# Optimization experiments

Hardware: AMD Instinct MI355X
Metric: run time of the kernel (lower is better)

The kernel has to match this reference:

```python
import jax, jax.numpy as jnp
from jax import lax
import numpy as np

GZ = 15.0   # grid extent (float, from gz=15.0)
G = 15      # grid cells per axis


def _disty(p):
    # p: [B, N, 3] points in [0, GZ). 12 features per point:
    # offsets to cell center / lower corner / upper corner (9) + their euclidean norms (3)
    c = jnp.floor(jnp.clip(p, 0.0, GZ - 1e-4))
    off_c = p - (c + 0.5)
    off_l = p - c
    off_u = p - (c + 1.0)
    norms = jnp.stack([jnp.sqrt((o * o).sum(-1)) for o in (off_c, off_l, off_u)], axis=-1)
    return jnp.concatenate([off_c, off_l, off_u, norms], axis=-1)  # [B, N, 12]


def _mlp(x, W1, b1, W2, b2, W3, b3):
    h = jax.nn.elu(x @ W1 + b1)
    h = jax.nn.elu(h @ W2 + b2)
    return h @ W3 + b3  # [B, N, 4]


def _agg(feats, p):
    # scatter-max per-point features into the [G,G,G] grid of each scene
    B, N, C = feats.shape
    cell = jnp.floor(jnp.clip(p, 0.0, GZ - 1e-4)).astype(jnp.int32)  # [B, N, 3]
    flat = (cell[..., 0] * G + cell[..., 1]) * G + cell[..., 2]
    flat = flat + (jnp.arange(B, dtype=jnp.int32) * (G ** 3))[:, None]
    grid = jnp.zeros((B * G ** 3, C), feats.dtype)
    grid = grid.at[flat.reshape(-1)].max(feats.reshape(-1, C))
    return grid.reshape(B, G, G, G, C).transpose(0, 4, 1, 2, 3)  # [B, 4, G, G, G]


def _conv_bn_elu(x, w, b, g, beta, stride):
    y = lax.conv_general_dilated(x, w, (stride,) * 3, [(2, 2)] * 3,
                                 dimension_numbers=('NCDHW', 'OIDHW', 'NCDHW'))
    y = y + b[None, :, None, None, None]
    # BatchNorm3d, training mode (batch statistics), eps=1e-5
    m = y.mean((0, 2, 3, 4), keepdims=True)
    v = ((y - m) ** 2).mean((0, 2, 3, 4), keepdims=True)
    y = (y - m) * lax.rsqrt(v + 1e-5)
    y = y * g[None, :, None, None, None] + beta[None, :, None, None, None]
    return jax.nn.elu(y)


def setup_inputs():
    key = jax.random.key(0)
    ks = jax.random.split(key, 16)
    B, N = 4, 300000
    pts = lambda k: jax.random.uniform(k, (B, N, 3), jnp.float32, 0.0, GZ)
    lin = lambda k, i, o: (jax.random.normal(k, (i, o), jnp.float32) / np.sqrt(i)).astype(jnp.float32)
    inp = {
        'goals': pts(ks[0]), 'inputs': pts(ks[1]), 'backgrounds': pts(ks[2]),
        'W1': lin(ks[3], 12, 16), 'b1': jnp.zeros((16,), jnp.float32),
        'W2': lin(ks[4], 16, 16), 'b2': jnp.zeros((16,), jnp.float32),
        'W3': lin(ks[5], 16, 4),  'b3': jnp.zeros((4,), jnp.float32),
        'conv1_w': (jax.random.normal(ks[6], (8, 12, 5, 5, 5), jnp.float32) / np.sqrt(12 * 125)).astype(jnp.float32),
        'conv1_b': jnp.zeros((8,), jnp.float32),
        'bn1_g': jnp.ones((8,), jnp.float32), 'bn1_b': jnp.zeros((8,), jnp.float32),
        'convs_w': (jax.random.normal(ks[7], (6, 8, 8, 5, 5, 5), jnp.float32) / np.sqrt(8 * 125)).astype(jnp.float32),
        'convs_b': jnp.zeros((6, 8), jnp.float32),
        'bns_g': jnp.ones((6, 8), jnp.float32), 'bns_b': jnp.zeros((6, 8), jnp.float32),
    }
    return inp


def reference(goals, inputs, backgrounds, W1, b1, W2, b2, W3, b3,
              conv1_w, conv1_b, bn1_g, bn1_b, convs_w, convs_b, bns_g, bns_b):
    def encode(p):
        return _agg(_mlp(_disty(p), W1, b1, W2, b2, W3, b3), p)

    scenes = jnp.concatenate([encode(inputs), encode(goals), encode(backgrounds)], axis=1)  # [B,12,G,G,G]
    x = _conv_bn_elu(scenes, conv1_w, conv1_b, bn1_g, bn1_b, 2)  # [B,8,8,8,8]
    for i in range(6):
        x = _conv_bn_elu(x, convs_w[i], convs_b[i], bns_g[i], bns_b[i], 1)
    return x
```

## Files before the change

kernel.cpp:

```cpp
#include <hip/hip_runtime.h>
#include <math.h>

#define B 4
#define NPTS 300000
#define G 15
#define G3 3375
#define PAIR_FLOATS (4*G3)
#define SCENE_FLOATS (B*12*G3)

__device__ __forceinline__ float eluf(float v) {
    return v > 0.0f ? v : __expf(v) - 1.0f;
}

__global__ __launch_bounds__(256)
void mlp_kernel(const float* __restrict__ P0,
                const float* __restrict__ P1,
                const float* __restrict__ P2,
                const float* __restrict__ W1, const float* __restrict__ b1,
                const float* __restrict__ W2, const float* __restrict__ b2,
                const float* __restrict__ W3, const float* __restrict__ b3,
                float4* __restrict__ vals, int* __restrict__ cells,
                int s0, int m)
{
    int b   = blockIdx.y;
    int set = blockIdx.z;
    int i   = blockIdx.x * 256 + threadIdx.x;
    if (i >= m) return;
    const float* P = (set == 0) ? P0 : ((set == 1) ? P1 : P2);

    const float* p = P + ((size_t)b * NPTS + (size_t)(s0 + i)) * 3;
    float px = p[0], py = p[1], pz = p[2];

    const float HI = 14.9999f;
    float cx = floorf(fminf(fmaxf(px, 0.0f), HI));
    float cy = floorf(fminf(fmaxf(py, 0.0f), HI));
    float cz = floorf(fminf(fmaxf(pz, 0.0f), HI));

    float x[12];
    x[0] = px - (cx + 0.5f); x[1] = py - (cy + 0.5f); x[2] = pz - (cz + 0.5f);
    x[3] = px - cx;          x[4] = py - cy;          x[5] = pz - cz;
    x[6] = px - (cx + 1.0f); x[7] = py - (cy + 1.0f); x[8] = pz - (cz + 1.0f);
    x[9]  = sqrtf(x[0]*x[0] + x[1]*x[1] + x[2]*x[2]);
    x[10] = sqrtf(x[3]*x[3] + x[4]*x[4] + x[5]*x[5]);
    x[11] = sqrtf(x[6]*x[6] + x[7]*x[7] + x[8]*x[8]);

    float h1[16];
#pragma unroll
    for (int j = 0; j < 16; ++j) {
        float s = b1[j];
#pragma unroll
        for (int k = 0; k < 12; ++k) s = fmaf(x[k], W1[k*16 + j], s);
        h1[j] = eluf(s);
    }
    float h2[16];
#pragma unroll
    for (int j = 0; j < 16; ++j) {
        float s = b2[j];
#pragma unroll
        for (int k = 0; k < 16; ++k) s = fmaf(h1[k], W2[k*16 + j], s);
        h2[j] = eluf(s);
    }
    float o[4];
#pragma unroll
    for (int j = 0; j < 4; ++j) {
        float s = b3[j];
#pragma unroll
        for (int k = 0; k < 16; ++k) s = fmaf(h2[k], W3[k*4 + j], s);
        o[j] = s;
    }

    int cell = (((int)cx) * G + (int)cy) * G + (int)cz;
    int pair = b * 3 + set;
    vals [(size_t)pair * m + i] = make_float4(o[0], o[1], o[2], o[3]);
    cells[(size_t)pair * m + i] = cell;
}

__global__ __launch_bounds__(256)
void scatter_kernel(const float4* __restrict__ vals,
                    const int* __restrict__ cells,
                    float* __restrict__ scenesR, int K, int m, int carry)
{
    __shared__ unsigned sg[PAIR_FLOATS];

    int rep = blockIdx.x;
    int b   = blockIdx.y;
    int set = blockIdx.z;
    int pair = b * 3 + set;
    float* myrep = scenesR + ((size_t)pair * K + rep) * PAIR_FLOATS;

    if (carry) {
        for (int i = threadIdx.x; i < PAIR_FLOATS; i += 256)
            sg[i] = __float_as_uint(myrep[i]);
    } else {
        for (int i = threadIdx.x; i < PAIR_FLOATS; i += 256)
            sg[i] = 0u;
    }
    __syncthreads();

    int chunk = (m + K - 1) / K;
    int start = rep * chunk;
    int end   = min(m, start + chunk);
    const float4* v = vals  + (size_t)pair * m;
    const int*    c = cells + (size_t)pair * m;

    for (int i = start + (int)threadIdx.x; i < end; i += 256) {
        float4 o = v[i];
        int cell = c[i];
        if (o.x > 0.0f) atomicMax(&sg[          cell], __float_as_uint(o.x));
        if (o.y > 0.0f) atomicMax(&sg[    G3 + cell], __float_as_uint(o.y));
        if (o.z > 0.0f) atomicMax(&sg[2 * G3 + cell], __float_as_uint(o.z));
        if (o.w > 0.0f) atomicMax(&sg[3 * G3 + cell], __float_as_uint(o.w));
    }
    __syncthreads();

    for (int i = threadIdx.x; i < PAIR_FLOATS; i += 256)
        myrep[i] = __uint_as_float(sg[i]);
}

__global__ __launch_bounds__(256)
void reduce_kernel(const float* __restrict__ scenesR, float* __restrict__ scenes,
                   int K)
{
    int t = blockIdx.x * 256 + threadIdx.x;
    if (t >= SCENE_FLOATS) return;
    int pair = t / PAIR_FLOATS;
    int j    = t - pair * PAIR_FLOATS;
    const float* src = scenesR + (size_t)pair * K * PAIR_FLOATS + j;
    float mx = 0.0f;
    for (int r = 0; r < K; ++r)
        mx = fmaxf(mx, src[(size_t)r * PAIR_FLOATS]);
    scenes[t] = mx;
}

__global__ __launch_bounds__(256)
void conv1_kernel(const float* __restrict__ scenes,
                  const float* __restrict__ w,
                  const float* __restrict__ bias,
                  float* __restrict__ y, float* __restrict__ stats)
{
    __shared__ float sred[256];
    int bx = blockIdx.x;
    int od = bx & 7, co = (bx >> 3) & 7, b = bx >> 6;
    int tid = threadIdx.x;
    int ow = tid & 7, oh = (tid >> 3) & 7, ciq = tid >> 6;

    float s = 0.0f;
    for (int cin = 0; cin < 3; ++cin) {
        int ci = ciq * 3 + cin;
        const float* sc = scenes + (size_t)(b * 12 + ci) * G3;
        const float* wc = w + (size_t)(co * 12 + ci) * 125;
#pragma unroll
        for (int kd = 0; kd < 5; ++kd) {
            int id = od * 2 - 2 + kd;
            if ((unsigned)id >= (unsigned)G) continue;
#pragma unroll
            for (int kh = 0; kh < 5; ++kh) {
                int ih = oh * 2 - 2 + kh;
                bool hok = (unsigned)ih < (unsigned)G;
#pragma unroll
                for (int kw = 0; kw < 5; ++kw) {
                    int iw = ow * 2 - 2 + kw;
                    if (hok && (unsigned)iw < (unsigned)G)
                        s = fmaf(sc[(id * G + ih) * G + iw], wc[kd*25 + kh*5 + kw], s);
                }
            }
        }
    }
    sred[tid] = s;
    __syncthreads();
    if (tid < 64) {
        float tot = sred[tid] + sred[64+tid] + sred[128+tid] + sred[192+tid] + bias[co];
        y[(size_t)(b * 8 + co) * 512 + od * 64 + tid] = tot;
        float sum = tot, sq = tot * tot;
#pragma unroll
        for (int o = 32; o > 0; o >>= 1) {
            sum += __shfl_down(sum, o, 64);
            sq  += __shfl_down(sq,  o, 64);
        }
        if (tid == 0) { atomicAdd(&stats[co], sum); atomicAdd(&stats[8 + co], sq); }
    }
}

__global__ __launch_bounds__(256)
void conv_s_kernel(const float* __restrict__ yin,
                   const float* __restrict__ w,
                   const float* __restrict__ bias,
                   const float* __restrict__ g, const float* __restrict__ bet,
                   const float* __restrict__ stats_in,
                   float* __restrict__ yout, float* __restrict__ stats_out)
{
    __shared__ float slab[8 * 5 * 144];
    __shared__ float sscale[8], sshift[8];
    __shared__ float sred[256];

    int bx = blockIdx.x;
    int od = bx & 7, co = (bx >> 3) & 7, b = bx >> 6;
    int tid = threadIdx.x;

    if (tid < 8) {
        float S = stats_in[tid], Q = stats_in[8 + tid];
        float m  = S * (1.0f / 2048.0f);
        float vv = Q * (1.0f / 2048.0f) - m * m;
        float rs = rsqrtf(vv + 1e-5f);
        float sc = g[tid] * rs;
        sscale[tid] = sc;
        sshift[tid] = bet[tid] - m * sc;
    }
    __syncthreads();

    for (int s = tid; s < 5760; s += 256) {
        int ci = s / 720; int r = s % 720;
        int kd = r / 144; int r2 = r % 144;
        int ph = r2 / 12, pw = r2 % 12;
        int id = od - 2 + kd, ih = ph - 2, iw = pw - 2;
        float v = 0.0f;
        if ((unsigned)id < 8u && (unsigned)ih < 8u && (unsigned)iw < 8u) {
            float raw = yin[(size_t)(b * 8 + ci) * 512 + id * 64 + ih * 8 + iw];
            float t = fmaf(raw, sscale[ci], sshift[ci]);
            v = t > 0.0f ? t : __expf(t) - 1.0f;
        }
        slab[s] = v;
    }
    __syncthreads();

    int ow = tid & 7, oh = (tid >> 3) & 7, ciq = tid >> 6;
    float s = 0.0f;
#pragma unroll
    for (int c2 = 0; c2 < 2; ++c2) {
        int ci = ciq * 2 + c2;
        const float* sl = slab + ci * 720;
        const float* wc = w + (size_t)(co * 8 + ci) * 125;
#pragma unroll
        for (int kd = 0; kd < 5; ++kd) {
#pragma unroll
            for (int kh = 0; kh < 5; ++kh) {
                const float* row = sl + kd * 144 + (oh + kh) * 12 + ow;
                const float* wr = wc + kd * 25 + kh * 5;
#pragma unroll
                for (int kw = 0; kw < 5; ++kw) s = fmaf(row[kw], wr[kw], s);
            }
        }
    }
    sred[tid] = s;
    __syncthreads();
    if (tid < 64) {
        float tot = sred[tid] + sred[64+tid] + sred[128+tid] + sred[192+tid] + bias[co];
        yout[(size_t)(b * 8 + co) * 512 + od * 64 + tid] = tot;
        float sum = tot, sq = tot * tot;
#pragma unroll
        for (int o = 32; o > 0; o >>= 1) {
            sum += __shfl_down(sum, o, 64);
            sq  += __shfl_down(sq,  o, 64);
        }
        if (tid == 0) { atomicAdd(&stats_out[co], sum); atomicAdd(&stats_out[8 + co], sq); }
    }
}

__global__ __launch_bounds__(256)
void bn_final_kernel(const float* __restrict__ yin,
                     const float* __restrict__ g, const float* __restrict__ bet,
                     const float* __restrict__ stats_in, float* __restrict__ outp)
{
    int i = blockIdx.x * 256 + threadIdx.x;
    int c = (i >> 9) & 7;
    float S = stats_in[c], Q = stats_in[8 + c];
    float m  = S * (1.0f / 2048.0f);
    float vv = Q * (1.0f / 2048.0f) - m * m;
    float rs = rsqrtf(vv + 1e-5f);
    float sc = g[c] * rs;
    float sh = bet[c] - m * sc;
    float t = fmaf(yin[i], sc, sh);
    outp[i] = t > 0.0f ? t : __expf(t) - 1.0f;
}

extern "C" void kernel_launch(void* const* d_in, const int* in_sizes, int n_in,
                              void* d_out, int out_size, void* d_ws, size_t ws_size,
                              hipStream_t stream)
{
    const float* goals       = (const float*)d_in[0];
    const float* inputs      = (const float*)d_in[1];
    const float* backgrounds = (const float*)d_in[2];
    const float* W1 = (const float*)d_in[3];
    const float* b1 = (const float*)d_in[4];
    const float* W2 = (const float*)d_in[5];
    const float* b2 = (const float*)d_in[6];
    const float* W3 = (const float*)d_in[7];
    const float* b3 = (const float*)d_in[8];
    const float* conv1_w = (const float*)d_in[9];
    const float* conv1_b = (const float*)d_in[10];
    const float* bn1_g   = (const float*)d_in[11];
    const float* bn1_b   = (const float*)d_in[12];
    const float* convs_w = (const float*)d_in[13];
    const float* convs_b = (const float*)d_in[14];
    const float* bns_g   = (const float*)d_in[15];
    const float* bns_b   = (const float*)d_in[16];

    long ws_floats = (long)(ws_size / 4);
    long fixed = SCENE_FLOATS + 2L * 16384 + 112;
    static const int plans[][2] = {
        {42,1},{42,2},{42,4},{24,4},{21,6},{16,8},{8,12},{4,16},{2,32},{1,64}};
    int K = 1, S = 64;
    for (int pi = 0; pi < 10; ++pi) {
        int pk = plans[pi][0], ps = plans[pi][1];
        long mseg = (NPTS + ps - 1) / ps;
        long need = 60L * mseg + (long)pk * SCENE_FLOATS + fixed;
        if (need <= ws_floats) { K = pk; S = ps; break; }
    }
    int Mseg = (NPTS + S - 1) / S;

    float*  wsp     = (float*)d_ws;
    float4* vals    = (float4*)wsp;
    int*    cells   = (int*)(wsp + 48L * Mseg);
    float*  scenesR = wsp + 60L * Mseg;
    float*  scenes  = scenesR + (size_t)K * SCENE_FLOATS;
    float*  yA      = scenes + SCENE_FLOATS;
    float*  yB      = yA + 16384;
    float*  stats   = yB + 16384;

    hipMemsetAsync(stats, 0, 7 * 16 * sizeof(float), stream);

    for (int s = 0; s < S; ++s) {
        int s0 = s * Mseg;
        int m  = min(Mseg, NPTS - s0);
        dim3 agrid((m + 255) / 256, B, 3);
        mlp_kernel<<<agrid, 256, 0, stream>>>(inputs, goals, backgrounds,
                                              W1, b1, W2, b2, W3, b3,
                                              vals, cells, s0, m);
        dim3 bgrid(K, B, 3);
        scatter_kernel<<<bgrid, 256, 0, stream>>>(vals, cells, scenesR, K, m,
                                                  s > 0 ? 1 : 0);
    }

    reduce_kernel<<<(SCENE_FLOATS + 255) / 256, 256, 0, stream>>>(scenesR, scenes, K);

    conv1_kernel<<<256, 256, 0, stream>>>(scenes, conv1_w, conv1_b, yA, stats);

    const float* cur = yA;
    float* nxt = yB;
    for (int i = 0; i < 6; ++i) {
        const float* g   = (i == 0) ? bn1_g : (bns_g + (i - 1) * 8);
        const float* bet = (i == 0) ? bn1_b : (bns_b + (i - 1) * 8);
        conv_s_kernel<<<256, 256, 0, stream>>>(
            cur, convs_w + (size_t)i * 8000, convs_b + i * 8,
            g, bet, stats + i * 16, nxt, stats + (i + 1) * 16);
        const float* tmp = cur; cur = nxt; nxt = (float*)tmp;
    }

    bn_final_kernel<<<64, 256, 0, stream>>>(cur, bns_g + 5 * 8, bns_b + 5 * 8,
                                            stats + 6 * 16, (float*)d_out);
}
```

Measured before the change: 327.4 us.

## Fuse reduce, conv chain and final BN into one cooperative kernel

Replaces the reduce, conv1, six conv_s and final BN launches with a single cooperative kernel that uses grid-wide syncs between stages. This removes about eight kernel launches and their inter-kernel gaps on the small tail of the pipeline. It relies on all 256 blocks being co-resident, and grid.sync costs stand in for the launch boundaries. The MLP/scatter stage, which dominates the runtime, is unchanged.

```diff
diff --git a/kernel.cpp b/kernel.cpp
--- a/kernel.cpp
+++ b/kernel.cpp
@@ -1,5 +1,8 @@
 #include <hip/hip_runtime.h>
+#include <hip/hip_cooperative_groups.h>
 #include <math.h>
+
+namespace cg = cooperative_groups;
 
 #define B 4
 #define NPTS 300000
@@ -118,159 +121,162 @@
 }
 
 __global__ __launch_bounds__(256)
-void reduce_kernel(const float* __restrict__ scenesR, float* __restrict__ scenes,
-                   int K)
+void conv_chain_kernel(const float* __restrict__ scenesR, float* __restrict__ scenes,
+                       const float* __restrict__ c1w,
+                       const float* __restrict__ c1b,
+                       const float* __restrict__ csw,
+                       const float* __restrict__ csb,
+                       const float* __restrict__ bn1_g, const float* __restrict__ bn1_b,
+                       const float* __restrict__ bns_g, const float* __restrict__ bns_b,
+                       float* __restrict__ yA, float* __restrict__ yB,
+                       float* __restrict__ stats, float* __restrict__ outp, int K)
 {
-    int t = blockIdx.x * 256 + threadIdx.x;
-    if (t >= SCENE_FLOATS) return;
-    int pair = t / PAIR_FLOATS;
-    int j    = t - pair * PAIR_FLOATS;
-    const float* src = scenesR + (size_t)pair * K * PAIR_FLOATS + j;
-    float mx = 0.0f;
-    for (int r = 0; r < K; ++r)
-        mx = fmaxf(mx, src[(size_t)r * PAIR_FLOATS]);
-    scenes[t] = mx;
-}
-
-__global__ __launch_bounds__(256)
-void conv1_kernel(const float* __restrict__ scenes,
-                  const float* __restrict__ w,
-                  const float* __restrict__ bias,
-                  float* __restrict__ y, float* __restrict__ stats)
-{
-    __shared__ float sred[256];
-    int bx = blockIdx.x;
-    int od = bx & 7, co = (bx >> 3) & 7, b = bx >> 6;
-    int tid = threadIdx.x;
-    int ow = tid & 7, oh = (tid >> 3) & 7, ciq = tid >> 6;
-
-    float s = 0.0f;
-    for (int cin = 0; cin < 3; ++cin) {
-        int ci = ciq * 3 + cin;
-        const float* sc = scenes + (size_t)(b * 12 + ci) * G3;
-        const float* wc = w + (size_t)(co * 12 + ci) * 125;
-#pragma unroll
-        for (int kd = 0; kd < 5; ++kd) {
-            int id = od * 2 - 2 + kd;
-            if ((unsigned)id >= (unsigned)G) continue;
-#pragma unroll
-            for (int kh = 0; kh < 5; ++kh) {
-                int ih = oh * 2 - 2 + kh;
-                bool hok = (unsigned)ih < (unsigned)G;
-#pragma unroll
-                for (int kw = 0; kw < 5; ++kw) {
-                    int iw = ow * 2 - 2 + kw;
-                    if (hok && (unsigned)iw < (unsigned)G)
-                        s = fmaf(sc[(id * G + ih) * G + iw], wc[kd*25 + kh*5 + kw], s);
-                }
-            }
-        }
-    }
-    sred[tid] = s;
-    __syncthreads();
-    if (tid < 64) {
-        float tot = sred[tid] + sred[64+tid] + sred[128+tid] + sred[192+tid] + bias[co];
-        y[(size_t)(b * 8 + co) * 512 + od * 64 + tid] = tot;
-        float sum = tot, sq = tot * tot;
-#pragma unroll
-        for (int o = 32; o > 0; o >>= 1) {
-            sum += __shfl_down(sum, o, 64);
-            sq  += __shfl_down(sq,  o, 64);
-        }
-        if (tid == 0) { atomicAdd(&stats[co], sum); atomicAdd(&stats[8 + co], sq); }
-    }
-}
-
-__global__ __launch_bounds__(256)
-void conv_s_kernel(const float* __restrict__ yin,
-                   const float* __restrict__ w,
-                   const float* __restrict__ bias,
-                   const float* __restrict__ g, const float* __restrict__ bet,
-                   const float* __restrict__ stats_in,
-                   float* __restrict__ yout, float* __restrict__ stats_out)
-{
+    cg::grid_group gridg = cg::this_grid();
+
     __shared__ float slab[8 * 5 * 144];
     __shared__ float sscale[8], sshift[8];
     __shared__ float sred[256];
 
-    int bx = blockIdx.x;
+    int bx  = blockIdx.x;
+    int tid = threadIdx.x;
+    int gtid = bx * 256 + tid;
     int od = bx & 7, co = (bx >> 3) & 7, b = bx >> 6;
-    int tid = threadIdx.x;
-
-    if (tid < 8) {
-        float S = stats_in[tid], Q = stats_in[8 + tid];
+
+    for (int t = gtid; t < SCENE_FLOATS; t += 256 * 256) {
+        int pair = t / PAIR_FLOATS;
+        int j    = t - pair * PAIR_FLOATS;
+        const float* src = scenesR + (size_t)pair * K * PAIR_FLOATS + j;
+        float mx = 0.0f;
+        for (int r = 0; r < K; ++r)
+            mx = fmaxf(mx, src[(size_t)r * PAIR_FLOATS]);
+        scenes[t] = mx;
+    }
+    gridg.sync();
+
+    {
+        int ow = tid & 7, oh = (tid >> 3) & 7, ciq = tid >> 6;
+        float s = 0.0f;
+        for (int cin = 0; cin < 3; ++cin) {
+            int ci = ciq * 3 + cin;
+            const float* sc = scenes + (size_t)(b * 12 + ci) * G3;
+            const float* wc = c1w + (size_t)(co * 12 + ci) * 125;
+#pragma unroll
+            for (int kd = 0; kd < 5; ++kd) {
+                int id = od * 2 - 2 + kd;
+                if ((unsigned)id >= (unsigned)G) continue;
+#pragma unroll
+                for (int kh = 0; kh < 5; ++kh) {
+                    int ih = oh * 2 - 2 + kh;
+                    bool hok = (unsigned)ih < (unsigned)G;
+#pragma unroll
+                    for (int kw = 0; kw < 5; ++kw) {
+                        int iw = ow * 2 - 2 + kw;
+                        if (hok && (unsigned)iw < (unsigned)G)
+                            s = fmaf(sc[(id * G + ih) * G + iw], wc[kd*25 + kh*5 + kw], s);
+                    }
+                }
+            }
+        }
+        sred[tid] = s;
+        __syncthreads();
+        if (tid < 64) {
+            float tot = sred[tid] + sred[64+tid] + sred[128+tid] + sred[192+tid] + c1b[co];
+            yA[(size_t)(b * 8 + co) * 512 + od * 64 + tid] = tot;
+            float sum = tot, sq = tot * tot;
+#pragma unroll
+            for (int o = 32; o > 0; o >>= 1) {
+                sum += __shfl_down(sum, o, 64);
+                sq  += __shfl_down(sq,  o, 64);
+            }
+            if (tid == 0) { atomicAdd(&stats[co], sum); atomicAdd(&stats[8 + co], sq); }
+        }
+    }
+    gridg.sync();
+
+    float* cur = yA;
+    float* nxt = yB;
+    for (int layer = 0; layer < 6; ++layer) {
+        const float* g        = (layer == 0) ? bn1_g : (bns_g + (layer - 1) * 8);
+        const float* bet      = (layer == 0) ? bn1_b : (bns_b + (layer - 1) * 8);
+        const float* stats_in = stats + layer * 16;
+        float*      stats_out = stats + (layer + 1) * 16;
+        const float* w        = csw + (size_t)layer * 8000;
+        const float* bias     = csb + layer * 8;
+
+        if (tid < 8) {
+            float S = stats_in[tid], Q = stats_in[8 + tid];
+            float m  = S * (1.0f / 2048.0f);
+            float vv = Q * (1.0f / 2048.0f) - m * m;
+            float rs = rsqrtf(vv + 1e-5f);
+            float sc = g[tid] * rs;
+            sscale[tid] = sc;
+            sshift[tid] = bet[tid] - m * sc;
+        }
+        __syncthreads();
+
+        for (int s = tid; s < 5760; s += 256) {
+            int ci = s / 720; int r = s % 720;
+            int kd = r / 144; int r2 = r % 144;
+            int ph = r2 / 12, pw = r2 % 12;
+            int id = od - 2 + kd, ih = ph - 2, iw = pw - 2;
+            float v = 0.0f;
+            if ((unsigned)id < 8u && (unsigned)ih < 8u && (unsigned)iw < 8u) {
+                float raw = cur[(size_t)(b * 8 + ci) * 512 + id * 64 + ih * 8 + iw];
+                float t = fmaf(raw, sscale[ci], sshift[ci]);
+                v = t > 0.0f ? t : __expf(t) - 1.0f;
+            }
+            slab[s] = v;
+        }
+        __syncthreads();
+
+        int ow = tid & 7, oh = (tid >> 3) & 7, ciq = tid >> 6;
+        float s = 0.0f;
+#pragma unroll
+        for (int c2 = 0; c2 < 2; ++c2) {
+            int ci = ciq * 2 + c2;
+            const float* sl = slab + ci * 720;
+            const float* wc = w + (size_t)(co * 8 + ci) * 125;
+#pragma unroll
+            for (int kd = 0; kd < 5; ++kd) {
+#pragma unroll
+                for (int kh = 0; kh < 5; ++kh) {
+                    const float* row = sl + kd * 144 + (oh + kh) * 12 + ow;
+                    const float* wr = wc + kd * 25 + kh * 5;
+#pragma unroll
+                    for (int kw = 0; kw < 5; ++kw) s = fmaf(row[kw], wr[kw], s);
+                }
+            }
+        }
+        sred[tid] = s;
+        __syncthreads();
+        if (tid < 64) {
+            float tot = sred[tid] + sred[64+tid] + sred[128+tid] + sred[192+tid] + bias[co];
+            nxt[(size_t)(b * 8 + co) * 512 + od * 64 + tid] = tot;
+            float sum = tot, sq = tot * tot;
+#pragma unroll
+            for (int o = 32; o > 0; o >>= 1) {
+                sum += __shfl_down(sum, o, 64);
+                sq  += __shfl_down(sq,  o, 64);
+            }
+            if (tid == 0) { atomicAdd(&stats_out[co], sum); atomicAdd(&stats_out[8 + co], sq); }
+        }
+        gridg.sync();
+        float* tmp = cur; cur = nxt; nxt = tmp;
+        __syncthreads();
+    }
+
+    if (gtid < 16384) {
+        const float* stats_in = stats + 6 * 16;
+        int c = (gtid >> 9) & 7;
+        float S = stats_in[c], Q = stats_in[8 + c];
         float m  = S * (1.0f / 2048.0f);
         float vv = Q * (1.0f / 2048.0f) - m * m;
         float rs = rsqrtf(vv + 1e-5f);
-        float sc = g[tid] * rs;
-        sscale[tid] = sc;
-        sshift[tid] = bet[tid] - m * sc;
-    }
-    __syncthreads();
-
-    for (int s = tid; s < 5760; s += 256) {
-        int ci = s / 720; int r = s % 720;
-        int kd = r / 144; int r2 = r % 144;
-        int ph = r2 / 12, pw = r2 % 12;
-        int id = od - 2 + kd, ih = ph - 2, iw = pw - 2;
-        float v = 0.0f;
-        if ((unsigned)id < 8u && (unsigned)ih < 8u && (unsigned)iw < 8u) {
-            float raw = yin[(size_t)(b * 8 + ci) * 512 + id * 64 + ih * 8 + iw];
-            float t = fmaf(raw, sscale[ci], sshift[ci]);
-            v = t > 0.0f ? t : __expf(t) - 1.0f;
-        }
-        slab[s] = v;
-    }
-    __syncthreads();
-
-    int ow = tid & 7, oh = (tid >> 3) & 7, ciq = tid >> 6;
-    float s = 0.0f;
-#pragma unroll
-    for (int c2 = 0; c2 < 2; ++c2) {
-        int ci = ciq * 2 + c2;
-        const float* sl = slab + ci * 720;
-        const float* wc = w + (size_t)(co * 8 + ci) * 125;
-#pragma unroll
-        for (int kd = 0; kd < 5; ++kd) {
-#pragma unroll
-            for (int kh = 0; kh < 5; ++kh) {
-                const float* row = sl + kd * 144 + (oh + kh) * 12 + ow;
-                const float* wr = wc + kd * 25 + kh * 5;
-#pragma unroll
-                for (int kw = 0; kw < 5; ++kw) s = fmaf(row[kw], wr[kw], s);
-            }
-        }
-    }
-    sred[tid] = s;
-    __syncthreads();
-    if (tid < 64) {
-        float tot = sred[tid] + sred[64+tid] + sred[128+tid] + sred[192+tid] + bias[co];
-        yout[(size_t)(b * 8 + co) * 512 + od * 64 + tid] = tot;
-        float sum = tot, sq = tot * tot;
-#pragma unroll
-        for (int o = 32; o > 0; o >>= 1) {
-            sum += __shfl_down(sum, o, 64);
-            sq  += __shfl_down(sq,  o, 64);
-        }
-        if (tid == 0) { atomicAdd(&stats_out[co], sum); atomicAdd(&stats_out[8 + co], sq); }
-    }
-}
-
-__global__ __launch_bounds__(256)
-void bn_final_kernel(const float* __restrict__ yin,
-                     const float* __restrict__ g, const float* __restrict__ bet,
-                     const float* __restrict__ stats_in, float* __restrict__ outp)
-{
-    int i = blockIdx.x * 256 + threadIdx.x;
-    int c = (i >> 9) & 7;
-    float S = stats_in[c], Q = stats_in[8 + c];
-    float m  = S * (1.0f / 2048.0f);
-    float vv = Q * (1.0f / 2048.0f) - m * m;
-    float rs = rsqrtf(vv + 1e-5f);
-    float sc = g[c] * rs;
-    float sh = bet[c] - m * sc;
-    float t = fmaf(yin[i], sc, sh);
-    outp[i] = t > 0.0f ? t : __expf(t) - 1.0f;
+        float sc = (bns_g + 5 * 8)[c] * rs;
+        float sh = (bns_b + 5 * 8)[c] - m * sc;
+        float t = fmaf(cur[gtid], sc, sh);
+        outp[gtid] = t > 0.0f ? t : __expf(t) - 1.0f;
+    }
 }
 
 extern "C" void kernel_launch(void* const* d_in, const int* in_sizes, int n_in,
@@ -331,21 +337,12 @@
                                                   s > 0 ? 1 : 0);
     }
 
-    reduce_kernel<<<(SCENE_FLOATS + 255) / 256, 256, 0, stream>>>(scenesR, scenes, K);
-
-    conv1_kernel<<<256, 256, 0, stream>>>(scenes, conv1_w, conv1_b, yA, stats);
-
-    const float* cur = yA;
-    float* nxt = yB;
-    for (int i = 0; i < 6; ++i) {
-        const float* g   = (i == 0) ? bn1_g : (bns_g + (i - 1) * 8);
-        const float* bet = (i == 0) ? bn1_b : (bns_b + (i - 1) * 8);
-        conv_s_kernel<<<256, 256, 0, stream>>>(
-            cur, convs_w + (size_t)i * 8000, convs_b + i * 8,
-            g, bet, stats + i * 16, nxt, stats + (i + 1) * 16);
-        const float* tmp = cur; cur = nxt; nxt = (float*)tmp;
-    }
-
-    bn_final_kernel<<<64, 256, 0, stream>>>(cur, bns_g + 5 * 8, bns_b + 5 * 8,
-                                            stats + 6 * 16, (float*)d_out);
-}
+    float* outp = (float*)d_out;
+    void* cargs[] = {
+        (void*)&scenesR, (void*)&scenes, (void*)&conv1_w, (void*)&conv1_b,
+        (void*)&convs_w, (void*)&convs_b, (void*)&bn1_g, (void*)&bn1_b,
+        (void*)&bns_g, (void*)&bns_b, (void*)&yA, (void*)&yB,
+        (void*)&stats, (void*)&outp, (void*)&K };
+    hipLaunchCooperativeKernel((void*)conv_chain_kernel, dim3(256), dim3(256),
+                               cargs, 0, stream);
+}
```

Result: slower. 541.8 us (+65.5%).

## Fuse conv tail layers into persistent kernel with grid barrier; widen scatter blocks

Applied to the files above, without the earlier changes.

Replaces the six per-layer conv kernels and the final BN kernel with a single persistent 32-block kernel. Each block handles one (batch, out-channel) pair across all depths and syncs layers through an atomic grid barrier. This removes several kernel launches and the final elementwise pass. The cost is less parallelism per layer and a reliance on all blocks being co-resident. The scatter kernel block size is also doubled to 512 threads.

```diff
diff --git a/kernel.cpp b/kernel.cpp
--- a/kernel.cpp
+++ b/kernel.cpp
@@ -75,7 +75,7 @@
     cells[(size_t)pair * m + i] = cell;
 }
 
-__global__ __launch_bounds__(256)
+__global__ __launch_bounds__(512)
 void scatter_kernel(const float4* __restrict__ vals,
                     const int* __restrict__ cells,
                     float* __restrict__ scenesR, int K, int m, int carry)
@@ -89,10 +89,10 @@
     float* myrep = scenesR + ((size_t)pair * K + rep) * PAIR_FLOATS;
 
     if (carry) {
-        for (int i = threadIdx.x; i < PAIR_FLOATS; i += 256)
+        for (int i = threadIdx.x; i < PAIR_FLOATS; i += 512)
             sg[i] = __float_as_uint(myrep[i]);
     } else {
-        for (int i = threadIdx.x; i < PAIR_FLOATS; i += 256)
+        for (int i = threadIdx.x; i < PAIR_FLOATS; i += 512)
             sg[i] = 0u;
     }
     __syncthreads();
@@ -103,7 +103,7 @@
     const float4* v = vals  + (size_t)pair * m;
     const int*    c = cells + (size_t)pair * m;
 
-    for (int i = start + (int)threadIdx.x; i < end; i += 256) {
+    for (int i = start + (int)threadIdx.x; i < end; i += 512) {
         float4 o = v[i];
         int cell = c[i];
         if (o.x > 0.0f) atomicMax(&sg[          cell], __float_as_uint(o.x));
@@ -113,7 +113,7 @@
     }
     __syncthreads();
 
-    for (int i = threadIdx.x; i < PAIR_FLOATS; i += 256)
+    for (int i = threadIdx.x; i < PAIR_FLOATS; i += 512)
         myrep[i] = __uint_as_float(sg[i]);
 }
 
@@ -182,95 +182,142 @@
 }
 
 __global__ __launch_bounds__(256)
-void conv_s_kernel(const float* __restrict__ yin,
-                   const float* __restrict__ w,
-                   const float* __restrict__ bias,
-                   const float* __restrict__ g, const float* __restrict__ bet,
-                   const float* __restrict__ stats_in,
-                   float* __restrict__ yout, float* __restrict__ stats_out)
-{
-    __shared__ float slab[8 * 5 * 144];
-    __shared__ float sscale[8], sshift[8];
+void tail32_kernel(const float* __restrict__ yA, float* __restrict__ yB,
+                   float* __restrict__ yC,
+                   const float* __restrict__ csw,
+                   const float* __restrict__ csb,
+                   const float* __restrict__ bn1_g, const float* __restrict__ bn1_b,
+                   const float* __restrict__ bns_g, const float* __restrict__ bns_b,
+                   float* __restrict__ stats, unsigned* __restrict__ bar,
+                   float* __restrict__ outp)
+{
+    __shared__ float slab[8 * 12 * 144];
     __shared__ float sred[256];
-
-    int bx = blockIdx.x;
-    int od = bx & 7, co = (bx >> 3) & 7, b = bx >> 6;
+    __shared__ float sfinal[512];
+    __shared__ float sstat[16], sscale[8], sshift[8];
+
     int tid = threadIdx.x;
-
-    if (tid < 8) {
-        float S = stats_in[tid], Q = stats_in[8 + tid];
+    int bx  = blockIdx.x;
+    int co = bx & 7, b = bx >> 3;
+
+    const float* yin = yA;
+    float* yout = yB;
+    unsigned gen = 0;
+
+    for (int layer = 0; layer < 6; ++layer) {
+        const float* g   = (layer == 0) ? bn1_g : (bns_g + (layer - 1) * 8);
+        const float* bet = (layer == 0) ? bn1_b : (bns_b + (layer - 1) * 8);
+        const float* stats_in  = stats + layer * 16;
+        float*       stats_out = stats + (layer + 1) * 16;
+        const float* w = csw + (size_t)layer * 8000;
+
+        if (tid < 16)
+            sstat[tid] = __hip_atomic_load(stats_in + tid, __ATOMIC_RELAXED,
+                                           __HIP_MEMORY_SCOPE_AGENT);
+        for (int i = tid; i < 8 * 12 * 144; i += 256) slab[i] = 0.0f;
+        __syncthreads();
+        if (tid < 8) {
+            float S = sstat[tid], Q = sstat[8 + tid];
+            float m  = S * (1.0f / 2048.0f);
+            float vv = Q * (1.0f / 2048.0f) - m * m;
+            float rs = rsqrtf(vv + 1e-5f);
+            float sc = g[tid] * rs;
+            sscale[tid] = sc;
+            sshift[tid] = bet[tid] - m * sc;
+        }
+        __syncthreads();
+
+        for (int s = tid; s < 4096; s += 256) {
+            int ci = s >> 9, r = s & 511;
+            int id = r >> 6, ih = (r >> 3) & 7, iw = r & 7;
+            const float* src = yin + ((size_t)(b * 8 + ci) << 9) + r;
+            float raw = (layer == 0)
+                ? *src
+                : __hip_atomic_load(src, __ATOMIC_RELAXED, __HIP_MEMORY_SCOPE_AGENT);
+            float t = fmaf(raw, sscale[ci], sshift[ci]);
+            slab[ci * 1728 + (id + 2) * 144 + (ih + 2) * 12 + (iw + 2)] =
+                t > 0.0f ? t : __expf(t) - 1.0f;
+        }
+        __syncthreads();
+
+        int ow = tid & 7, oh = (tid >> 3) & 7, ciq = tid >> 6;
+        float sum_acc = 0.0f, sq_acc = 0.0f;
+        for (int od = 0; od < 8; ++od) {
+            float s = 0.0f;
+#pragma unroll
+            for (int c2 = 0; c2 < 2; ++c2) {
+                int ci = ciq * 2 + c2;
+                const float* sl = slab + ci * 1728 + od * 144;
+                const float* wc = w + (size_t)(co * 8 + ci) * 125;
+#pragma unroll
+                for (int kd = 0; kd < 5; ++kd) {
+#pragma unroll
+                    for (int kh = 0; kh < 5; ++kh) {
+                        const float* row = sl + kd * 144 + (oh + kh) * 12 + ow;
+                        const float* wr = wc + kd * 25 + kh * 5;
+#pragma unroll
+                        for (int kw = 0; kw < 5; ++kw) s = fmaf(row[kw], wr[kw], s);
+                    }
+                }
+            }
+            sred[tid] = s;
+            __syncthreads();
+            if (tid < 64) {
+                float tot = sred[tid] + sred[64+tid] + sred[128+tid] + sred[192+tid]
+                          + csb[layer * 8 + co];
+                sfinal[od * 64 + tid] = tot;
+                sum_acc += tot;
+                sq_acc  += tot * tot;
+                if (layer < 5)
+                    __hip_atomic_store(yout + ((size_t)(b * 8 + co) << 9) + od * 64 + tid,
+                                       tot, __ATOMIC_RELAXED, __HIP_MEMORY_SCOPE_AGENT);
+            }
+            __syncthreads();
+        }
+        if (tid < 64) {
+#pragma unroll
+            for (int o = 32; o > 0; o >>= 1) {
+                sum_acc += __shfl_down(sum_acc, o, 64);
+                sq_acc  += __shfl_down(sq_acc,  o, 64);
+            }
+            if (tid == 0) {
+                atomicAdd(stats_out + co, sum_acc);
+                atomicAdd(stats_out + 8 + co, sq_acc);
+            }
+        }
+
+        ++gen;
+        __syncthreads();
+        if (tid == 0) {
+            __hip_atomic_fetch_add(bar, 1u, __ATOMIC_ACQ_REL, __HIP_MEMORY_SCOPE_AGENT);
+            while (__hip_atomic_load(bar, __ATOMIC_ACQUIRE, __HIP_MEMORY_SCOPE_AGENT)
+                   < 32u * gen)
+                __builtin_amdgcn_s_sleep(2);
+        }
+        __syncthreads();
+
+        if (layer == 0) { yin = yB; yout = yC; }
+        else { float* t_ = yout; yout = (float*)yin; yin = t_; }
+    }
+
+    if (tid < 16)
+        sstat[tid] = __hip_atomic_load(stats + 6 * 16 + tid, __ATOMIC_RELAXED,
+                                       __HIP_MEMORY_SCOPE_AGENT);
+    __syncthreads();
+    if (tid < 64) {
+        float S = sstat[co], Q = sstat[8 + co];
         float m  = S * (1.0f / 2048.0f);
         float vv = Q * (1.0f / 2048.0f) - m * m;
         float rs = rsqrtf(vv + 1e-5f);
-        float sc = g[tid] * rs;
-        sscale[tid] = sc;
-        sshift[tid] = bet[tid] - m * sc;
-    }
-    __syncthreads();
-
-    for (int s = tid; s < 5760; s += 256) {
-        int ci = s / 720; int r = s % 720;
-        int kd = r / 144; int r2 = r % 144;
-        int ph = r2 / 12, pw = r2 % 12;
-        int id = od - 2 + kd, ih = ph - 2, iw = pw - 2;
-        float v = 0.0f;
-        if ((unsigned)id < 8u && (unsigned)ih < 8u && (unsigned)iw < 8u) {
-            float raw = yin[(size_t)(b * 8 + ci) * 512 + id * 64 + ih * 8 + iw];
-            float t = fmaf(raw, sscale[ci], sshift[ci]);
-            v = t > 0.0f ? t : __expf(t) - 1.0f;
-        }
-        slab[s] = v;
-    }
-    __syncthreads();
-
-    int ow = tid & 7, oh = (tid >> 3) & 7, ciq = tid >> 6;
-    float s = 0.0f;
-#pragma unroll
-    for (int c2 = 0; c2 < 2; ++c2) {
-        int ci = ciq * 2 + c2;
-        const float* sl = slab + ci * 720;
-        const float* wc = w + (size_t)(co * 8 + ci) * 125;
-#pragma unroll
-        for (int kd = 0; kd < 5; ++kd) {
-#pragma unroll
-            for (int kh = 0; kh < 5; ++kh) {
-                const float* row = sl + kd * 144 + (oh + kh) * 12 + ow;
-                const float* wr = wc + kd * 25 + kh * 5;
-#pragma unroll
-                for (int kw = 0; kw < 5; ++kw) s = fmaf(row[kw], wr[kw], s);
-            }
-        }
-    }
-    sred[tid] = s;
-    __syncthreads();
-    if (tid < 64) {
-        float tot = sred[tid] + sred[64+tid] + sred[128+tid] + sred[192+tid] + bias[co];
-        yout[(size_t)(b * 8 + co) * 512 + od * 64 + tid] = tot;
-        float sum = tot, sq = tot * tot;
-#pragma unroll
-        for (int o = 32; o > 0; o >>= 1) {
-            sum += __shfl_down(sum, o, 64);
-            sq  += __shfl_down(sq,  o, 64);
-        }
-        if (tid == 0) { atomicAdd(&stats_out[co], sum); atomicAdd(&stats_out[8 + co], sq); }
-    }
-}
-
-__global__ __launch_bounds__(256)
-void bn_final_kernel(const float* __restrict__ yin,
-                     const float* __restrict__ g, const float* __restrict__ bet,
-                     const float* __restrict__ stats_in, float* __restrict__ outp)
-{
-    int i = blockIdx.x * 256 + threadIdx.x;
-    int c = (i >> 9) & 7;
-    float S = stats_in[c], Q = stats_in[8 + c];
-    float m  = S * (1.0f / 2048.0f);
-    float vv = Q * (1.0f / 2048.0f) - m * m;
-    float rs = rsqrtf(vv + 1e-5f);
-    float sc = g[c] * rs;
-    float sh = bet[c] - m * sc;
-    float t = fmaf(yin[i], sc, sh);
-    outp[i] = t > 0.0f ? t : __expf(t) - 1.0f;
+        float sc = (bns_g + 5 * 8)[co] * rs;
+        float sh = (bns_b + 5 * 8)[co] - m * sc;
+#pragma unroll
+        for (int od = 0; od < 8; ++od) {
+            float t = fmaf(sfinal[od * 64 + tid], sc, sh);
+            outp[((size_t)(b * 8 + co) << 9) + od * 64 + tid] =
+                t > 0.0f ? t : __expf(t) - 1.0f;
+        }
+    }
 }
 
 extern "C" void kernel_launch(void* const* d_in, const int* in_sizes, int n_in,
@@ -296,7 +343,7 @@
     const float* bns_b   = (const float*)d_in[16];
 
     long ws_floats = (long)(ws_size / 4);
-    long fixed = SCENE_FLOATS + 2L * 16384 + 112;
+    long fixed = SCENE_FLOATS + 3L * 16384 + 128;
     static const int plans[][2] = {
         {42,1},{42,2},{42,4},{24,4},{21,6},{16,8},{8,12},{4,16},{2,32},{1,64}};
     int K = 1, S = 64;
@@ -308,16 +355,18 @@
     }
     int Mseg = (NPTS + S - 1) / S;
 
-    float*  wsp     = (float*)d_ws;
-    float4* vals    = (float4*)wsp;
-    int*    cells   = (int*)(wsp + 48L * Mseg);
-    float*  scenesR = wsp + 60L * Mseg;
-    float*  scenes  = scenesR + (size_t)K * SCENE_FLOATS;
-    float*  yA      = scenes + SCENE_FLOATS;
-    float*  yB      = yA + 16384;
-    float*  stats   = yB + 16384;
-
-    hipMemsetAsync(stats, 0, 7 * 16 * sizeof(float), stream);
+    float*    wsp     = (float*)d_ws;
+    float4*   vals    = (float4*)wsp;
+    int*      cells   = (int*)(wsp + 48L * Mseg);
+    float*    scenesR = wsp + 60L * Mseg;
+    float*    scenes  = scenesR + (size_t)K * SCENE_FLOATS;
+    float*    yA      = scenes + SCENE_FLOATS;
+    float*    yB      = yA + 16384;
+    float*    yC      = yB + 16384;
+    float*    stats   = yC + 16384;
+    unsigned* bar     = (unsigned*)(stats + 112);
+
+    hipMemsetAsync(stats, 0, 128 * sizeof(float), stream);
 
     for (int s = 0; s < S; ++s) {
         int s0 = s * Mseg;
@@ -327,7 +376,7 @@
                                               W1, b1, W2, b2, W3, b3,
                                               vals, cells, s0, m);
         dim3 bgrid(K, B, 3);
-        scatter_kernel<<<bgrid, 256, 0, stream>>>(vals, cells, scenesR, K, m,
+        scatter_kernel<<<bgrid, 512, 0, stream>>>(vals, cells, scenesR, K, m,
                                                   s > 0 ? 1 : 0);
     }
 
@@ -335,17 +384,7 @@
 
     conv1_kernel<<<256, 256, 0, stream>>>(scenes, conv1_w, conv1_b, yA, stats);
 
-    const float* cur = yA;
-    float* nxt = yB;
-    for (int i = 0; i < 6; ++i) {
-        const float* g   = (i == 0) ? bn1_g : (bns_g + (i - 1) * 8);
-        const float* bet = (i == 0) ? bn1_b : (bns_b + (i - 1) * 8);
-        conv_s_kernel<<<256, 256, 0, stream>>>(
-            cur, convs_w + (size_t)i * 8000, convs_b + i * 8,
-            g, bet, stats + i * 16, nxt, stats + (i + 1) * 16);
-        const float* tmp = cur; cur = nxt; nxt = (float*)tmp;
-    }
-
-    bn_final_kernel<<<64, 256, 0, stream>>>(cur, bns_g + 5 * 8, bns_b + 5 * 8,
-                                            stats + 6 * 16, (float*)d_out);
-}
+    tail32_kernel<<<32, 256, 0, stream>>>(yA, yB, yC, convs_w, convs_b,
+                                          bn1_g, bn1_b, bns_g, bns_b,
+                                          stats, bar, (float*)d_out);
+}
```

Measured after the change: 477.2 us. +45.8%, slower.
